# Performance work log

Measured on AMD Instinct MI355X. Metric: run time of the kernel, lower is better.

The kernel has to match this reference:

```python
import jax, jax.numpy as jnp
import numpy as np

B = 512    # batch of signals
N = 1024   # time samples per signal
M = 16384  # frequency grid points (super-resolved)


def setup_inputs() -> dict:
    key = jax.random.key(0)
    x = jax.random.normal(key, (B, 2, N), dtype=jnp.float32)  # [B, 2(re/im), N]
    xgrid = jnp.linspace(-0.5, 0.5, M, dtype=jnp.float32)      # normalized freqs
    return {"x": x, "xgrid": xgrid}


def reference(x, xgrid):
    # x: [B, 2, N] -> complex signal a + i*b
    # Periodogram at arbitrary freqs f: P(f) = |sum_n x_n * exp(-2j*pi*f*n)|^2 / N
    a = x[:, 0]  # real part [B, N]
    b = x[:, 1]  # imag part [B, N]
    Nn = x.shape[-1]
    n = jnp.arange(Nn, dtype=x.dtype)
    phase = (2.0 * jnp.pi) * xgrid[:, None] * n[None, :]  # [M, N]
    C = jnp.cos(phase)  # [M, N]
    S = jnp.sin(phase)  # [M, N]
    # x_n * (cos - i sin) = (a c + b s) + i (b c - a s)
    re = jnp.einsum('bn,mn->bm', a, C) + jnp.einsum('bn,mn->bm', b, S)
    im = jnp.einsum('bn,mn->bm', b, C) - jnp.einsum('bn,mn->bm', a, S)
    return (re * re + im * im) / Nn  # [B, M]
```

## Files before the change

### kernel.cpp

```cpp
#include <hip/hip_runtime.h>


typedef __fp16 half8  __attribute__((ext_vector_type(8)));
typedef __fp16 half2v __attribute__((ext_vector_type(2)));
typedef float  f32x4  __attribute__((ext_vector_type(4)));

#define B_SZ 512
#define N_SZ 1024
#define M_SZ 16384
#define KT 32
#define NT (N_SZ / KT)
#define WS_ARR 1048576

union U4 { half2v h2[4]; uint4 u; };
union BF { half2v h2[4]; half8 v; uint4 u; };

__device__ __forceinline__ void gld16(const void* g, void* l) {
    __builtin_amdgcn_global_load_lds((__attribute__((address_space(1))) void*)g,
                                     (__attribute__((address_space(3))) void*)l,
                                     16, 0, 0);
}

__global__ __launch_bounds__(256)
void cvt_kernel(const float* __restrict__ x, unsigned char* __restrict__ ws) {
    const int id  = (int)blockIdx.x * 256 + (int)threadIdx.x;
    const int arr = id >> 16;
    const int rem = id & 65535;
    const int rb  = rem >> 11;
    const int kc  = (rem >> 6) & 31;
    const int l6  = rem & 63;
    const int r16 = l6 >> 2;
    const int g   = l6 & 3;
    const float* src = x + (size_t)(rb * 16 + r16) * 2048 + arr * 1024 + kc * 32 + g * 8;
    const float4 v0 = *(const float4*)src;
    const float4 v1 = *(const float4*)(src + 4);
    U4 u;
    u.h2[0] = __builtin_amdgcn_cvt_pkrtz(v0.x, v0.y);
    u.h2[1] = __builtin_amdgcn_cvt_pkrtz(v0.z, v0.w);
    u.h2[2] = __builtin_amdgcn_cvt_pkrtz(v1.x, v1.y);
    u.h2[3] = __builtin_amdgcn_cvt_pkrtz(v1.z, v1.w);
    *(uint4*)(ws + (size_t)arr * WS_ARR + (size_t)(rb * 32 + kc) * 1024 + (g * 16 + r16) * 16) = u.u;
}

__global__ __launch_bounds__(256, 4)
void periodogram_kernel(const unsigned char* __restrict__ ws,
                        const float* __restrict__ xgrid,
                        float* __restrict__ out) {
    __shared__ __align__(16) unsigned char smem[32768];
    const int tid  = (int)threadIdx.x;
    const int lane = tid & 63;
    const int w    = tid >> 6;
    const int bid  = (int)blockIdx.x;
    const int b0 = (bid & 7) * 64;
    const int m0 = (bid >> 3) * 64;

    const int wr = (w >> 1) * 32;
    const int wc = (w & 1) * 32;

    unsigned char* lb = smem + (unsigned)(w * 8192);
    const int l15 = lane & 15;

    const unsigned char* pA[2];
#pragma unroll
    for (int fm = 0; fm < 2; ++fm) {
        const int rb = ((b0 + wr) >> 4) + fm;
        pA[fm] = ws + (size_t)(rb * 32) * 1024 + (size_t)(lane * 16);
    }

    half2v PC[2][4], PS[2][4];
    float c0v[2], s0v[2], C32[2], S32[2];
    const float g8f = (float)((lane >> 4) << 3);
#pragma unroll
    for (int fn = 0; fn < 2; ++fn) {
        const float xg = xgrid[m0 + wc + fn * 16 + l15];
        float Cj[8], Sj[8];
        Cj[0] = 1.0f; Sj[0] = 0.0f;
#pragma unroll
        for (int j = 1; j < 8; ++j) {
            float p = xg * (float)j; p -= floorf(p);
            Cj[j] = __builtin_amdgcn_cosf(p);
            Sj[j] = __builtin_amdgcn_sinf(p);
        }
#pragma unroll
        for (int i = 0; i < 4; ++i) {
            PC[fn][i] = __builtin_amdgcn_cvt_pkrtz(Cj[2 * i], Cj[2 * i + 1]);
            PS[fn][i] = __builtin_amdgcn_cvt_pkrtz(Sj[2 * i], Sj[2 * i + 1]);
        }
        float p32 = xg * 32.0f; p32 -= floorf(p32);
        C32[fn] = __builtin_amdgcn_cosf(p32);
        S32[fn] = __builtin_amdgcn_sinf(p32);
        float pb = xg * g8f; pb -= floorf(pb);
        c0v[fn] = __builtin_amdgcn_cosf(pb);
        s0v[fn] = __builtin_amdgcn_sinf(pb);
    }

    f32x4 accRe[2][2], accIm[2][2];
#pragma unroll
    for (int i = 0; i < 2; ++i)
#pragma unroll
        for (int j = 0; j < 2; ++j) { accRe[i][j] = (f32x4)0.0f; accIm[i][j] = (f32x4)0.0f; }

#pragma unroll
    for (int fm = 0; fm < 2; ++fm) {
        gld16(pA[fm], lb + (unsigned)(fm * 1024));
        gld16(pA[fm] + WS_ARR, lb + (unsigned)(2048 + fm * 1024));
    }

    for (int t = 0; t < NT; ++t) {
        const unsigned cb = (unsigned)(t & 1) * 4096u;
        asm volatile("s_waitcnt vmcnt(0)" ::: "memory");
        half8 fa[2], fb[2];
#pragma unroll
        for (int fm = 0; fm < 2; ++fm) {
            fa[fm] = *(const half8*)(lb + cb + (unsigned)(fm * 1024) + (unsigned)(lane * 16));
            fb[fm] = *(const half8*)(lb + cb + (unsigned)(2048 + fm * 1024) + (unsigned)(lane * 16));
        }
        if (t < NT - 1) {
            const unsigned nb = cb ^ 4096u;
            const unsigned off = (unsigned)((t + 1) * 1024);
#pragma unroll
            for (int fm = 0; fm < 2; ++fm) {
                gld16(pA[fm] + off, lb + nb + (unsigned)(fm * 1024));
                gld16(pA[fm] + WS_ARR + off, lb + nb + (unsigned)(2048 + fm * 1024));
            }
        }
#pragma unroll
        for (int fn = 0; fn < 2; ++fn) {
            const float c0 = c0v[fn], s0 = s0v[fn];
            const half2v c0b = __builtin_amdgcn_cvt_pkrtz(c0, c0);
            const half2v s0b = __builtin_amdgcn_cvt_pkrtz(s0, s0);
            BF fc, fs, fns;
#pragma unroll
            for (int i = 0; i < 4; ++i) {
                fc.h2[i] = c0b * PC[fn][i] - s0b * PS[fn][i];
                fs.h2[i] = s0b * PC[fn][i] + c0b * PS[fn][i];
            }
            __builtin_amdgcn_s_setprio(1);
#pragma unroll
            for (int fm = 0; fm < 2; ++fm) {
                accRe[fm][fn] = __builtin_amdgcn_mfma_f32_16x16x32_f16(fa[fm], fc.v, accRe[fm][fn], 0, 0, 0);
                accIm[fm][fn] = __builtin_amdgcn_mfma_f32_16x16x32_f16(fb[fm], fc.v, accIm[fm][fn], 0, 0, 0);
            }
            fns.u.x = fs.u.x ^ 0x80008000u;
            fns.u.y = fs.u.y ^ 0x80008000u;
            fns.u.z = fs.u.z ^ 0x80008000u;
            fns.u.w = fs.u.w ^ 0x80008000u;
#pragma unroll
            for (int fm = 0; fm < 2; ++fm) {
                accRe[fm][fn] = __builtin_amdgcn_mfma_f32_16x16x32_f16(fb[fm], fs.v,  accRe[fm][fn], 0, 0, 0);
                accIm[fm][fn] = __builtin_amdgcn_mfma_f32_16x16x32_f16(fa[fm], fns.v, accIm[fm][fn], 0, 0, 0);
            }
            __builtin_amdgcn_s_setprio(0);
            c0v[fn] = __builtin_fmaf(c0, C32[fn], -(s0 * S32[fn]));
            s0v[fn] = __builtin_fmaf(s0, C32[fn],  (c0 * S32[fn]));
        }
    }

    const float inv = 1.0f / (float)N_SZ;
    const int orow0 = b0 + wr + ((lane >> 4) << 2);
    const int ocol0 = m0 + wc + l15;
#pragma unroll
    for (int fm = 0; fm < 2; ++fm)
#pragma unroll
        for (int fn = 0; fn < 2; ++fn) {
            const f32x4 r = accRe[fm][fn];
            const f32x4 im = accIm[fm][fn];
            const int col = ocol0 + fn * 16;
#pragma unroll
            for (int j = 0; j < 4; ++j) {
                const int row = orow0 + fm * 16 + j;
                out[(size_t)row * M_SZ + col] = (r[j] * r[j] + im[j] * im[j]) * inv;
            }
        }
}

extern "C" void kernel_launch(void* const* d_in, const int* in_sizes, int n_in,
                              void* d_out, int out_size, void* d_ws, size_t ws_size,
                              hipStream_t stream) {
    const float* x     = (const float*)d_in[0];
    const float* xgrid = (const float*)d_in[1];
    float* out = (float*)d_out;
    unsigned char* ws = (unsigned char*)d_ws;
    cvt_kernel<<<512, 256, 0, stream>>>(x, ws);
    dim3 grid(8 * (M_SZ / 64));
    dim3 block(256);
    periodogram_kernel<<<grid, block, 0, stream>>>(ws, xgrid, out);
}
```

Baseline: 80.27 us.

## Enlarge per-wave batch tile and load A fragments directly into registers

Each wave now covers 128 batch rows instead of 32, so block tile grows to 256x64 and the grid shrinks fourfold. This reuses the generated twiddle (cos/sin) fragments across more MFMAs, amortizing the per-k-step VALU twiddle rotation. The LDS double-buffered async global-to-LDS path is removed in favor of direct global loads into registers each step. Accumulators grow to 64 f32x4 registers per lane, lowering occupancy (launch bounds 2), and loads are no longer prefetched ahead, risking exposed memory latency.

```diff
diff --git a/kernel.cpp b/kernel.cpp
--- a/kernel.cpp
+++ b/kernel.cpp
@@ -14,12 +14,6 @@
 
 union U4 { half2v h2[4]; uint4 u; };
 union BF { half2v h2[4]; half8 v; uint4 u; };
-
-__device__ __forceinline__ void gld16(const void* g, void* l) {
-    __builtin_amdgcn_global_load_lds((__attribute__((address_space(1))) void*)g,
-                                     (__attribute__((address_space(3))) void*)l,
-                                     16, 0, 0);
-}
 
 __global__ __launch_bounds__(256)
 void cvt_kernel(const float* __restrict__ x, unsigned char* __restrict__ ws) {
@@ -42,30 +36,22 @@
     *(uint4*)(ws + (size_t)arr * WS_ARR + (size_t)(rb * 32 + kc) * 1024 + (g * 16 + r16) * 16) = u.u;
 }
 
-__global__ __launch_bounds__(256, 4)
+__global__ __launch_bounds__(256, 2)
 void periodogram_kernel(const unsigned char* __restrict__ ws,
                         const float* __restrict__ xgrid,
                         float* __restrict__ out) {
-    __shared__ __align__(16) unsigned char smem[32768];
     const int tid  = (int)threadIdx.x;
     const int lane = tid & 63;
     const int w    = tid >> 6;
     const int bid  = (int)blockIdx.x;
-    const int b0 = (bid & 7) * 64;
-    const int m0 = (bid >> 3) * 64;
+    const int b0 = (bid & 1) * 256;
+    const int m0 = (bid >> 1) * 64;
 
-    const int wr = (w >> 1) * 32;
+    const int wr = (w >> 1) * 128;
     const int wc = (w & 1) * 32;
-
-    unsigned char* lb = smem + (unsigned)(w * 8192);
     const int l15 = lane & 15;
 
-    const unsigned char* pA[2];
-#pragma unroll
-    for (int fm = 0; fm < 2; ++fm) {
-        const int rb = ((b0 + wr) >> 4) + fm;
-        pA[fm] = ws + (size_t)(rb * 32) * 1024 + (size_t)(lane * 16);
-    }
+    const unsigned char* pA0 = ws + (size_t)(((b0 + wr) >> 4) * 32) * 1024 + (size_t)(lane * 16);
 
     half2v PC[2][4], PS[2][4];
     float c0v[2], s0v[2], C32[2], S32[2];
@@ -94,35 +80,19 @@
         s0v[fn] = __builtin_amdgcn_sinf(pb);
     }
 
-    f32x4 accRe[2][2], accIm[2][2];
+    f32x4 accRe[8][2], accIm[8][2];
 #pragma unroll
-    for (int i = 0; i < 2; ++i)
+    for (int i = 0; i < 8; ++i)
 #pragma unroll
         for (int j = 0; j < 2; ++j) { accRe[i][j] = (f32x4)0.0f; accIm[i][j] = (f32x4)0.0f; }
 
+    for (int t = 0; t < NT; ++t) {
+        half8 fa[8], fb[8];
+        const unsigned off = (unsigned)(t * 1024);
 #pragma unroll
-    for (int fm = 0; fm < 2; ++fm) {
-        gld16(pA[fm], lb + (unsigned)(fm * 1024));
-        gld16(pA[fm] + WS_ARR, lb + (unsigned)(2048 + fm * 1024));
-    }
-
-    for (int t = 0; t < NT; ++t) {
-        const unsigned cb = (unsigned)(t & 1) * 4096u;
-        asm volatile("s_waitcnt vmcnt(0)" ::: "memory");
-        half8 fa[2], fb[2];
-#pragma unroll
-        for (int fm = 0; fm < 2; ++fm) {
-            fa[fm] = *(const half8*)(lb + cb + (unsigned)(fm * 1024) + (unsigned)(lane * 16));
-            fb[fm] = *(const half8*)(lb + cb + (unsigned)(2048 + fm * 1024) + (unsigned)(lane * 16));
-        }
-        if (t < NT - 1) {
-            const unsigned nb = cb ^ 4096u;
-            const unsigned off = (unsigned)((t + 1) * 1024);
-#pragma unroll
-            for (int fm = 0; fm < 2; ++fm) {
-                gld16(pA[fm] + off, lb + nb + (unsigned)(fm * 1024));
-                gld16(pA[fm] + WS_ARR + off, lb + nb + (unsigned)(2048 + fm * 1024));
-            }
+        for (int fm = 0; fm < 8; ++fm) {
+            fa[fm] = *(const half8*)(pA0 + (unsigned)(fm * 32768) + off);
+            fb[fm] = *(const half8*)(pA0 + WS_ARR + (unsigned)(fm * 32768) + off);
         }
 #pragma unroll
         for (int fn = 0; fn < 2; ++fn) {
@@ -137,7 +107,7 @@
             }
             __builtin_amdgcn_s_setprio(1);
 #pragma unroll
-            for (int fm = 0; fm < 2; ++fm) {
+            for (int fm = 0; fm < 8; ++fm) {
                 accRe[fm][fn] = __builtin_amdgcn_mfma_f32_16x16x32_f16(fa[fm], fc.v, accRe[fm][fn], 0, 0, 0);
                 accIm[fm][fn] = __builtin_amdgcn_mfma_f32_16x16x32_f16(fb[fm], fc.v, accIm[fm][fn], 0, 0, 0);
             }
@@ -146,7 +116,7 @@
             fns.u.z = fs.u.z ^ 0x80008000u;
             fns.u.w = fs.u.w ^ 0x80008000u;
 #pragma unroll
-            for (int fm = 0; fm < 2; ++fm) {
+            for (int fm = 0; fm < 8; ++fm) {
                 accRe[fm][fn] = __builtin_amdgcn_mfma_f32_16x16x32_f16(fb[fm], fs.v,  accRe[fm][fn], 0, 0, 0);
                 accIm[fm][fn] = __builtin_amdgcn_mfma_f32_16x16x32_f16(fa[fm], fns.v, accIm[fm][fn], 0, 0, 0);
             }
@@ -160,7 +130,7 @@
     const int orow0 = b0 + wr + ((lane >> 4) << 2);
     const int ocol0 = m0 + wc + l15;
 #pragma unroll
-    for (int fm = 0; fm < 2; ++fm)
+    for (int fm = 0; fm < 8; ++fm)
 #pragma unroll
         for (int fn = 0; fn < 2; ++fn) {
             const f32x4 r = accRe[fm][fn];
@@ -182,7 +152,7 @@
     float* out = (float*)d_out;
     unsigned char* ws = (unsigned char*)d_ws;
     cvt_kernel<<<512, 256, 0, stream>>>(x, ws);
-    dim3 grid(8 * (M_SZ / 64));
+    dim3 grid(2 * (M_SZ / 64));
     dim3 block(256);
     periodogram_kernel<<<grid, block, 0, stream>>>(ws, xgrid, out);
 }
```

Result: faster. 68.42 us (-14.8%).
